# Kernel tuning notes

Hardware: AMD Instinct MI355X
Metric: run time of the kernel (lower is better)

## Reference

```python
import jax, jax.numpy as jnp
import numpy as np

B = 16384          # batch size (positions)
NNZ_PER = 32       # active features per position (pieces on board)
F = 768            # 2 colors x 6 pieces x 64 squares
H = 512            # hidden_size


def setup_inputs() -> dict:
    key = jax.random.key(0)
    k1, k2, k3, k4, k5, k6 = jax.random.split(key, 6)
    nnz = B * NNZ_PER
    batch_row = jnp.repeat(jnp.arange(B, dtype=jnp.int64), NNZ_PER)
    stm_feat = jax.random.randint(k1, (nnz,), 0, F, dtype=jnp.int64)
    nstm_feat = jax.random.randint(k2, (nnz,), 0, F, dtype=jnp.int64)
    stm_indices = jnp.stack([batch_row, stm_feat])    # [2, nnz] COO (batch, feature)
    nstm_indices = jnp.stack([batch_row, nstm_feat])  # [2, nnz]
    stm_values = jnp.ones((nnz,), dtype=jnp.float32)   # binary features
    nstm_values = jnp.ones((nnz,), dtype=jnp.float32)
    W_ft = jax.random.normal(k3, (H, F), dtype=jnp.float32) * 0.02
    b_ft = jax.random.normal(k4, (H,), dtype=jnp.float32) * 0.02
    W_out = jax.random.normal(k5, (1, 2 * H), dtype=jnp.float32) * 0.02
    b_out = jax.random.normal(k6, (1,), dtype=jnp.float32) * 0.02
    return {
        "stm_indices": stm_indices,
        "nstm_indices": nstm_indices,
        "stm_values": stm_values,
        "nstm_values": nstm_values,
        "batch_size": B,
        "W_ft": W_ft,
        "b_ft": b_ft,
        "W_out": W_out,
        "b_out": b_out,
    }


def _to_dense(indices, values, batch_size):
    # torch.sparse_coo_tensor(...).to_dense(): duplicates are summed.
    dense = jnp.zeros((batch_size, F), dtype=jnp.float32)
    return dense.at[indices[0], indices[1]].add(values)


def reference(stm_indices, nstm_indices, stm_values, nstm_values, batch_size,
              W_ft, b_ft, W_out, b_out):
    stm_dense = _to_dense(stm_indices, stm_values, batch_size)     # [B, 768]
    nstm_dense = _to_dense(nstm_indices, nstm_values, batch_size)  # [B, 768]
    stm_hidden = stm_dense @ W_ft.T + b_ft     # [B, H]
    nstm_hidden = nstm_dense @ W_ft.T + b_ft   # [B, H]
    hidden = jnp.concatenate([stm_hidden, nstm_hidden], axis=1)  # [B, 2H]
    hidden = jnp.clip(hidden, 0.0, 1.0)
    return jax.nn.sigmoid(hidden @ W_out.T + b_out)  # [B, 1]
```

## Files before the change

kernel.cpp:

```cpp
#include <hip/hip_runtime.h>
#include <hip/hip_fp16.h>

#define B_SZ    16384
#define NNZ_PER 32
#define F_DIM   768
#define H_DIM   512

typedef unsigned int  uint32;
typedef unsigned long long uint64;
typedef unsigned char uchar;

__device__ inline uchar f32_to_e5m2(float x) {
    __half h = __float2half_rn(x);
    unsigned short hb = *(unsigned short*)&h;
    unsigned short lsb = (hb >> 8) & 1;
    hb = (unsigned short)(hb + 0x7F + lsb);
    return (uchar)(hb >> 8);
}

__global__ __launch_bounds__(256) void transpose_convert(
    const float* __restrict__ W, uchar* __restrict__ Wt8)
{
    __shared__ float tile[32][33];
    const int f0 = blockIdx.x * 32;
    const int h0 = blockIdx.y * 32;
    const int tx = threadIdx.x;
    const int ty = threadIdx.y;

#pragma unroll
    for (int i = 0; i < 32; i += 8)
        tile[ty + i][tx] = W[(h0 + ty + i) * F_DIM + f0 + tx];
    __syncthreads();
#pragma unroll
    for (int i = 0; i < 32; i += 8)
        Wt8[(size_t)(f0 + ty + i) * H_DIM + h0 + tx] = f32_to_e5m2(tile[tx][ty + i]);
}

__global__ __launch_bounds__(256, 6) void nnue_fwd(
    const int*   __restrict__ stm_idx,
    const int*   __restrict__ nstm_idx,
    const float* __restrict__ stm_val,
    const float* __restrict__ nstm_val,
    const uchar* __restrict__ Wt8,
    const float* __restrict__ b_ft,
    const float* __restrict__ W_out,
    const float* __restrict__ b_out,
    float* __restrict__ out)
{
    const int tid  = threadIdx.x;
    const int w    = tid >> 6;
    const int pos  = w >> 1;
    const int hh   = w & 1;
    const int lane = tid & 63;
    const int half = lane >> 5;
    const int c    = lane & 31;
    const int b    = blockIdx.x * 2 + pos;
    const int NNZ  = B_SZ * NNZ_PER;

    __shared__ uint64 sh[2][64];
    __shared__ float  pdot[2][2];

    if (tid < 128) {
        const int p    = tid >> 6;
        const int s    = tid & 63;
        const int base = (blockIdx.x * 2 + p) * NNZ_PER;
        int f; float v;
        if (s < 32) { f = stm_idx [NNZ + base + s];        v = stm_val [base + s]; }
        else        { f = nstm_idx[NNZ + base + (s - 32)]; v = nstm_val[base + (s - 32)]; }
        __half2 vv = __float2half2_rn(v);
        sh[p][s] = ((uint64)(*(uint32*)&vv) << 32) | (uint32)f;
    }
    __syncthreads();

    const uint32 selA = 0x01040004u;
    const uint32 selB = 0x03040204u;
    const uint32 coff = ((uint32)hh << 8) | ((uint32)c << 3);
    const char*  Wb   = (const char*)Wt8;

    __half2 z = __float2half2_rn(0.f);
    __half2 sa[4] = {z, z, z, z};
    __half2 na[4] = {z, z, z, z};

    uint2   bufA[8], bufB[8];
    __half2 valA[8], valB[8];

#define LOAD_GROUP(g, BUF, VAL)                                               \
    {                                                                         \
        _Pragma("unroll")                                                     \
        for (int i = 0; i < 8; ++i) {                                         \
            const int j = 4 * (g) + (i & 3);                                  \
            const int slot = (i < 4 ? 0 : 32) + 2 * j + half;                 \
            uint64 e  = sh[pos][slot];                                        \
            uint32 f  = (uint32)e;                                            \
            uint32 v2 = (uint32)(e >> 32);                                    \
            VAL[i] = *(__half2*)&v2;                                          \
            uint32 off = (f << 9) | coff;                                     \
            BUF[i] = *(const uint2*)(Wb + off);                               \
        }                                                                     \
    }

#define FMA_GROUP(BUF, VAL)                                                   \
    {                                                                         \
        _Pragma("unroll")                                                     \
        for (int i = 0; i < 8; ++i) {                                         \
            __half2* acc = (i < 4) ? sa : na;                                 \
            uint2 wv = BUF[i];                                                \
            __half2 vv = VAL[i];                                              \
            uint32 p;                                                         \
            p = __builtin_amdgcn_perm(0u, wv.x, selA); acc[0] = __hfma2(*(__half2*)&p, vv, acc[0]); \
            p = __builtin_amdgcn_perm(0u, wv.x, selB); acc[1] = __hfma2(*(__half2*)&p, vv, acc[1]); \
            p = __builtin_amdgcn_perm(0u, wv.y, selA); acc[2] = __hfma2(*(__half2*)&p, vv, acc[2]); \
            p = __builtin_amdgcn_perm(0u, wv.y, selB); acc[3] = __hfma2(*(__half2*)&p, vv, acc[3]); \
        }                                                                     \
    }

    LOAD_GROUP(0, bufA, valA);
    LOAD_GROUP(1, bufB, valB);
    FMA_GROUP(bufA, valA);
    LOAD_GROUP(2, bufA, valA);
    FMA_GROUP(bufB, valB);
    LOAD_GROUP(3, bufB, valB);
    FMA_GROUP(bufA, valA);
    FMA_GROUP(bufB, valB);

#undef LOAD_GROUP
#undef FMA_GROUP

    const float* bias = b_ft  + (hh << 8) + (c << 3);
    const float* wo   = W_out + half * H_DIM + (hh << 8) + (c << 3);
    float dot = 0.f;
#pragma unroll
    for (int k = 0; k < 4; ++k) {
        int ms = *(int*)&sa[k];
        int mn = *(int*)&na[k];
        int os = __shfl_xor(ms, 32, 64);
        int on = __shfl_xor(mn, 32, 64);
        int mm = half ? mn : ms;
        int oo = half ? on : os;
        __half2 mh = *(__half2*)&mm;
        __half2 oh = *(__half2*)&oo;
        float h0 = __low2float(mh)  + __low2float(oh);
        float h1 = __high2float(mh) + __high2float(oh);
        float a0 = fminf(fmaxf(h0 + bias[2 * k],     0.f), 1.f);
        float a1 = fminf(fmaxf(h1 + bias[2 * k + 1], 0.f), 1.f);
        dot += a0 * wo[2 * k] + a1 * wo[2 * k + 1];
    }

#pragma unroll
    for (int off = 32; off > 0; off >>= 1)
        dot += __shfl_xor(dot, off, 64);

    if (lane == 0)
        pdot[pos][hh] = dot;
    __syncthreads();

    if (hh == 0 && lane == 0) {
        float d = pdot[pos][0] + pdot[pos][1] + b_out[0];
        out[b] = 1.f / (1.f + expf(-d));
    }
}

extern "C" void kernel_launch(void* const* d_in, const int* in_sizes, int n_in,
                              void* d_out, int out_size, void* d_ws, size_t ws_size,
                              hipStream_t stream) {
    const int*   stm_idx  = (const int*)  d_in[0];
    const int*   nstm_idx = (const int*)  d_in[1];
    const float* stm_val  = (const float*)d_in[2];
    const float* nstm_val = (const float*)d_in[3];
    const float* W_ft     = (const float*)d_in[5];
    const float* b_ft     = (const float*)d_in[6];
    const float* W_out    = (const float*)d_in[7];
    const float* b_out    = (const float*)d_in[8];
    float*       out      = (float*)d_out;
    uchar*       Wt8      = (uchar*)d_ws;

    dim3 tb(32, 8);
    dim3 tg(F_DIM / 32, H_DIM / 32);
    transpose_convert<<<tg, tb, 0, stream>>>(W_ft, Wt8);

    nnue_fwd<<<B_SZ / 2, 256, 0, stream>>>(stm_idx, nstm_idx, stm_val, nstm_val,
                                           Wt8, b_ft, W_out, b_out, out);
}
```

Before: 109.4 us.

## Map one wave per position with 16-byte weight loads and no cross-wave reduction

Each 64-lane wave now handles a whole batch position across all 512 hidden units, instead of two waves splitting the hidden dimension. Each lane loads 16 FP8 weights per feature row with a uint4 access instead of 8, and feature metadata is read from shared memory with vector loads. The second __syncthreads and the shared-memory partial-dot combine are removed, and the grid shrinks to B/4 blocks. The cost is doubled per-lane accumulators and buffers, which raises register pressure and may limit occupancy under the launch bound of 6 waves.

```diff
diff --git a/kernel.cpp b/kernel.cpp
--- a/kernel.cpp
+++ b/kernel.cpp
@@ -49,88 +49,103 @@
 {
     const int tid  = threadIdx.x;
     const int w    = tid >> 6;
-    const int pos  = w >> 1;
-    const int hh   = w & 1;
     const int lane = tid & 63;
     const int half = lane >> 5;
     const int c    = lane & 31;
-    const int b    = blockIdx.x * 2 + pos;
+    const int b    = blockIdx.x * 4 + w;
     const int NNZ  = B_SZ * NNZ_PER;
 
-    __shared__ uint64 sh[2][64];
-    __shared__ float  pdot[2][2];
-
-    if (tid < 128) {
-        const int p    = tid >> 6;
-        const int s    = tid & 63;
-        const int base = (blockIdx.x * 2 + p) * NNZ_PER;
+    __shared__ uint64 sh[4][64];
+    {
+        const int base = b * NNZ_PER;
+        const int k    = lane & 31;
         int f; float v;
-        if (s < 32) { f = stm_idx [NNZ + base + s];        v = stm_val [base + s]; }
-        else        { f = nstm_idx[NNZ + base + (s - 32)]; v = nstm_val[base + (s - 32)]; }
+        if (lane < 32) { f = stm_idx [NNZ + base + k]; v = stm_val [base + k]; }
+        else           { f = nstm_idx[NNZ + base + k]; v = nstm_val[base + k]; }
+        const int side = lane >> 5;
+        const int idx  = (k & 1) * 32 + side * 16 + (k >> 1);
         __half2 vv = __float2half2_rn(v);
-        sh[p][s] = ((uint64)(*(uint32*)&vv) << 32) | (uint32)f;
+        sh[w][idx] = ((uint64)(*(uint32*)&vv) << 32) | (uint32)f;
     }
     __syncthreads();
 
     const uint32 selA = 0x01040004u;
     const uint32 selB = 0x03040204u;
-    const uint32 coff = ((uint32)hh << 8) | ((uint32)c << 3);
+    const uint32 coff = (uint32)c << 4;
     const char*  Wb   = (const char*)Wt8;
+    const uint64* meta = &sh[w][half * 32];
 
     __half2 z = __float2half2_rn(0.f);
-    __half2 sa[4] = {z, z, z, z};
-    __half2 na[4] = {z, z, z, z};
+    __half2 sa[8] = {z,z,z,z,z,z,z,z};
+    __half2 na[8] = {z,z,z,z,z,z,z,z};
 
-    uint2   bufA[8], bufB[8];
-    __half2 valA[8], valB[8];
+    uint4   bufA[4], bufB[4];
+    __half2 valA[4], valB[4];
 
 #define LOAD_GROUP(g, BUF, VAL)                                               \
     {                                                                         \
+        const int o = ((g) >= 4 ? 16 : 0) + 4 * ((g) & 3);                    \
+        ulonglong2 m0 = *(const ulonglong2*)(meta + o);                       \
+        ulonglong2 m1 = *(const ulonglong2*)(meta + o + 2);                   \
+        uint64 ee0 = m0.x, ee1 = m0.y, ee2 = m1.x, ee3 = m1.y;                \
+        uint64 ee[4] = {ee0, ee1, ee2, ee3};                                  \
         _Pragma("unroll")                                                     \
-        for (int i = 0; i < 8; ++i) {                                         \
-            const int j = 4 * (g) + (i & 3);                                  \
-            const int slot = (i < 4 ? 0 : 32) + 2 * j + half;                 \
-            uint64 e  = sh[pos][slot];                                        \
-            uint32 f  = (uint32)e;                                            \
-            uint32 v2 = (uint32)(e >> 32);                                    \
+        for (int i = 0; i < 4; ++i) {                                         \
+            uint32 f  = (uint32)ee[i];                                        \
+            uint32 v2 = (uint32)(ee[i] >> 32);                                \
             VAL[i] = *(__half2*)&v2;                                          \
-            uint32 off = (f << 9) | coff;                                     \
-            BUF[i] = *(const uint2*)(Wb + off);                               \
+            BUF[i] = *(const uint4*)(Wb + (((size_t)f) << 9) + coff);         \
         }                                                                     \
     }
 
-#define FMA_GROUP(BUF, VAL)                                                   \
+#define FMA_GROUP(BUF, VAL, ACC)                                              \
     {                                                                         \
         _Pragma("unroll")                                                     \
-        for (int i = 0; i < 8; ++i) {                                         \
-            __half2* acc = (i < 4) ? sa : na;                                 \
-            uint2 wv = BUF[i];                                                \
+        for (int i = 0; i < 4; ++i) {                                         \
+            uint4 wv = BUF[i];                                                \
             __half2 vv = VAL[i];                                              \
             uint32 p;                                                         \
-            p = __builtin_amdgcn_perm(0u, wv.x, selA); acc[0] = __hfma2(*(__half2*)&p, vv, acc[0]); \
-            p = __builtin_amdgcn_perm(0u, wv.x, selB); acc[1] = __hfma2(*(__half2*)&p, vv, acc[1]); \
-            p = __builtin_amdgcn_perm(0u, wv.y, selA); acc[2] = __hfma2(*(__half2*)&p, vv, acc[2]); \
-            p = __builtin_amdgcn_perm(0u, wv.y, selB); acc[3] = __hfma2(*(__half2*)&p, vv, acc[3]); \
+            p = __builtin_amdgcn_perm(0u, wv.x, selA); ACC[0] = __hfma2(*(__half2*)&p, vv, ACC[0]); \
+            p = __builtin_amdgcn_perm(0u, wv.x, selB); ACC[1] = __hfma2(*(__half2*)&p, vv, ACC[1]); \
+            p = __builtin_amdgcn_perm(0u, wv.y, selA); ACC[2] = __hfma2(*(__half2*)&p, vv, ACC[2]); \
+            p = __builtin_amdgcn_perm(0u, wv.y, selB); ACC[3] = __hfma2(*(__half2*)&p, vv, ACC[3]); \
+            p = __builtin_amdgcn_perm(0u, wv.z, selA); ACC[4] = __hfma2(*(__half2*)&p, vv, ACC[4]); \
+            p = __builtin_amdgcn_perm(0u, wv.z, selB); ACC[5] = __hfma2(*(__half2*)&p, vv, ACC[5]); \
+            p = __builtin_amdgcn_perm(0u, wv.w, selA); ACC[6] = __hfma2(*(__half2*)&p, vv, ACC[6]); \
+            p = __builtin_amdgcn_perm(0u, wv.w, selB); ACC[7] = __hfma2(*(__half2*)&p, vv, ACC[7]); \
         }                                                                     \
     }
 
     LOAD_GROUP(0, bufA, valA);
     LOAD_GROUP(1, bufB, valB);
-    FMA_GROUP(bufA, valA);
+    FMA_GROUP(bufA, valA, sa);
     LOAD_GROUP(2, bufA, valA);
-    FMA_GROUP(bufB, valB);
+    FMA_GROUP(bufB, valB, sa);
     LOAD_GROUP(3, bufB, valB);
-    FMA_GROUP(bufA, valA);
-    FMA_GROUP(bufB, valB);
+    FMA_GROUP(bufA, valA, sa);
+    LOAD_GROUP(4, bufA, valA);
+    FMA_GROUP(bufB, valB, sa);
+    LOAD_GROUP(5, bufB, valB);
+    FMA_GROUP(bufA, valA, na);
+    LOAD_GROUP(6, bufA, valA);
+    FMA_GROUP(bufB, valB, na);
+    LOAD_GROUP(7, bufB, valB);
+    FMA_GROUP(bufA, valA, na);
+    FMA_GROUP(bufB, valB, na);
 
 #undef LOAD_GROUP
 #undef FMA_GROUP
 
-    const float* bias = b_ft  + (hh << 8) + (c << 3);
-    const float* wo   = W_out + half * H_DIM + (hh << 8) + (c << 3);
+    const float4* b4 = (const float4*)(b_ft + c * 16);
+    const float4* w4 = (const float4*)(W_out + half * H_DIM + c * 16);
+    float4 bv[4] = {b4[0], b4[1], b4[2], b4[3]};
+    float4 wv4[4] = {w4[0], w4[1], w4[2], w4[3]};
+    const float* bias = (const float*)bv;
+    const float* wo   = (const float*)wv4;
+
     float dot = 0.f;
 #pragma unroll
-    for (int k = 0; k < 4; ++k) {
+    for (int k = 0; k < 8; ++k) {
         int ms = *(int*)&sa[k];
         int mn = *(int*)&na[k];
         int os = __shfl_xor(ms, 32, 64);
@@ -151,13 +166,7 @@
         dot += __shfl_xor(dot, off, 64);
 
     if (lane == 0)
-        pdot[pos][hh] = dot;
-    __syncthreads();
-
-    if (hh == 0 && lane == 0) {
-        float d = pdot[pos][0] + pdot[pos][1] + b_out[0];
-        out[b] = 1.f / (1.f + expf(-d));
-    }
+        out[b] = 1.f / (1.f + expf(-(dot + b_out[0])));
 }
 
 extern "C" void kernel_launch(void* const* d_in, const int* in_sizes, int n_in,
@@ -178,6 +187,6 @@
     dim3 tg(F_DIM / 32, H_DIM / 32);
     transpose_convert<<<tg, tb, 0, stream>>>(W_ft, Wt8);
 
-    nnue_fwd<<<B_SZ / 2, 256, 0, stream>>>(stm_idx, nstm_idx, stm_val, nstm_val,
+    nnue_fwd<<<B_SZ / 4, 256, 0, stream>>>(stm_idx, nstm_idx, stm_val, nstm_val,
                                            Wt8, b_ft, W_out, b_out, out);
 }
```

Measured after the change: 100.6 us. 1.09x faster.
